# Performance work log

Measured on AMD Instinct MI355X. Metric: run time of the kernel, lower is better.

## Reference

```python
import jax, jax.numpy as jnp
import numpy as np

B, N_SIGNALS, SIGNAL_LEN, H = 512, 3, 4096, 17

def setup_inputs() -> dict:
    key = jax.random.key(0)
    ks = jax.random.split(key, 11)
    s = 1.0 / np.sqrt(H)  # torch nn.RNN init scale
    return {
        "x": jax.random.normal(ks[0], (B, N_SIGNALS, SIGNAL_LEN), jnp.float32),
        "W_ih_f": jax.random.uniform(ks[1], (H, N_SIGNALS), jnp.float32, -s, s),
        "W_hh_f": jax.random.uniform(ks[2], (H, H), jnp.float32, -s, s),
        "b_ih_f": jax.random.uniform(ks[3], (H,), jnp.float32, -s, s),
        "b_hh_f": jax.random.uniform(ks[4], (H,), jnp.float32, -s, s),
        "W_ih_b": jax.random.uniform(ks[5], (H, N_SIGNALS), jnp.float32, -s, s),
        "W_hh_b": jax.random.uniform(ks[6], (H, H), jnp.float32, -s, s),
        "b_ih_b": jax.random.uniform(ks[7], (H,), jnp.float32, -s, s),
        "b_hh_b": jax.random.uniform(ks[8], (H,), jnp.float32, -s, s),
        "conv_w": jax.random.uniform(ks[9], (2, 2 * H), jnp.float32, -1.0 / np.sqrt(2 * H), 1.0 / np.sqrt(2 * H)),
        "conv_b": jax.random.uniform(ks[10], (2,), jnp.float32, -1.0 / np.sqrt(2 * H), 1.0 / np.sqrt(2 * H)),
    }

def _run_rnn(xt, W_ih, W_hh, b_ih, b_hh):
    # xt: [B, T, C] -> hs: [B, T, H]
    pre = jnp.einsum('btc,hc->bth', xt, W_ih) + b_ih + b_hh  # precompute input projection
    def step(h, p):
        h = jnp.tanh(p + h @ W_hh.T)
        return h, h
    h0 = jnp.zeros((xt.shape[0], W_hh.shape[0]), xt.dtype)
    _, hs = jax.lax.scan(step, h0, jnp.swapaxes(pre, 0, 1))
    return jnp.swapaxes(hs, 0, 1)

def reference(x, W_ih_f, W_hh_f, b_ih_f, b_hh_f, W_ih_b, W_hh_b, b_ih_b, b_hh_b, conv_w, conv_b):
    xt = jnp.transpose(x, (0, 2, 1))  # [B, T, N_SIGNALS]
    fwd = _run_rnn(xt, W_ih_f, W_hh_f, b_ih_f, b_hh_f)                      # [B, T, H]
    bwd = _run_rnn(xt[:, ::-1], W_ih_b, W_hh_b, b_ih_b, b_hh_b)[:, ::-1]    # [B, T, H]
    out = jnp.concatenate([fwd, bwd], axis=-1)                               # [B, T, 2H]
    logits_t = jnp.einsum('bth,oh->bto', out, conv_w) + conv_b               # 1x1 conv == per-step linear
    return jnp.mean(logits_t, axis=1)                                        # [B, 2]
```

## Files before the change

### kernel.cpp

```cpp
#include <hip/hip_runtime.h>

#define BATCH 512
#define NC 3
#define TT 4096
#define HH 17
#define NBLK (TT / 4)
#define WU_BLKS 3
#define NSEQ (BATCH * 2)
#define SCALE 2.8853900817779268f

typedef __attribute__((ext_vector_type(8))) short short8;
typedef __attribute__((ext_vector_type(16))) float f32x16;

union B8 { unsigned u[4]; short8 s; };

__device__ __forceinline__ float fast_exp2(float y) {
#if __has_builtin(__builtin_amdgcn_exp2f)
    return __builtin_amdgcn_exp2f(y);
#else
    return exp2f(y);
#endif
}

__device__ __forceinline__ float fast_tanh_pre(float d) {
    float e = fast_exp2(d);
    float r = __builtin_amdgcn_rcpf(e + 1.0f);
    return fmaf(-2.0f, r, 1.0f);
}

__device__ __forceinline__ unsigned cvt_pk_bf16(float lo, float hi) {
    unsigned r;
    asm("v_cvt_pk_bf16_f32 %0, %1, %2" : "=v"(r) : "v"(lo), "v"(hi));
    return r;
}

__device__ __forceinline__ unsigned short bf16_rne(float f) {
    unsigned u = __float_as_uint(f);
    unsigned r = u + 0x7FFFu + ((u >> 16) & 1u);
    return (unsigned short)(r >> 16);
}

__global__ __launch_bounds__(256) void transpose_kernel(
    const float4* __restrict__ x4, uint4* __restrict__ w12,
    uint4* __restrict__ w0) {
    __shared__ float4 tile[NC][32][33];
    int bid = blockIdx.x;
    int tb = bid & 15;
    int tt = bid >> 4;
    int b0 = tb * 32, t40 = tt * 32;
    int jr = threadIdx.x & 31, pr = threadIdx.x >> 5;
#pragma unroll
    for (int c = 0; c < NC; ++c)
#pragma unroll
        for (int p = 0; p < 4; ++p) {
            int r = p * 8 + pr;
            tile[c][r][jr] =
                x4[(size_t)(b0 + r) * (NC * NBLK) + c * NBLK + t40 + jr];
        }
    __syncthreads();
#pragma unroll
    for (int p = 0; p < 4; ++p) {
        int j = p * 8 + pr;
        int b = jr;
        float4 c0 = tile[0][b][j];
        float4 c1 = tile[1][b][j];
        float4 c2 = tile[2][b][j];
        uint4 a, z;
        a.x = cvt_pk_bf16(c1.x, c2.x); z.x = cvt_pk_bf16(0.0f, c0.x);
        a.y = cvt_pk_bf16(c1.y, c2.y); z.y = cvt_pk_bf16(0.0f, c0.y);
        a.z = cvt_pk_bf16(c1.z, c2.z); z.z = cvt_pk_bf16(0.0f, c0.z);
        a.w = cvt_pk_bf16(c1.w, c2.w); z.w = cvt_pk_bf16(0.0f, c0.w);
        size_t idx = (size_t)(t40 + j) * BATCH + b0 + b;
        w12[idx] = a;
        w0[idx] = z;
    }
}

template <int DIR>
__device__ __forceinline__ void run_loop(
    const uint4* __restrict__ p12, const uint4* __restrict__ p0,
    short8 Ahi, short8 Alo, short8 A2hi, short8 A2lo,
    f32x16 Cb, int g, int blk0, int blkMain, int blkEnd, float* hs) {

    short8 Bhi = {0,0,0,0,0,0,0,0};
    unsigned h16b = 0;

    int t4 = DIR ? (NBLK - 1 - blk0) : blk0;
    uint4 c12 = p12[(size_t)t4 * BATCH];
    uint4 c0 = p0[(size_t)t4 * BATCH];
    const int dstep = DIR ? -1 : 1;

    for (int blk = blk0; blk < blkEnd; ++blk) {
        int nt4 = (blk + 1 < blkEnd) ? t4 + dstep : t4;
        uint4 n12 = p12[(size_t)nt4 * BATCH];
        uint4 n0 = p0[(size_t)nt4 * BATCH];

        const float flag = (blk >= blkMain) ? 1.0f : 0.0f;
        unsigned a12[4] = {c12.x, c12.y, c12.z, c12.w};
        unsigned a0[4] = {c0.x, c0.y, c0.z, c0.w};

#pragma unroll
        for (int k = 0; k < 4; ++k) {
            const int kk = DIR ? (3 - k) : k;

            unsigned t0 = h16b | a0[kk];
            unsigned t1 = a12[kk];
            if (g) { t0 = 0; t1 = 0; }
            B8 th; th.u[0] = t0; th.u[1] = t1; th.u[2] = 0; th.u[3] = 0;

            f32x16 D = __builtin_amdgcn_mfma_f32_32x32x16_bf16(Ahi, Bhi, Cb, 0, 0, 0);
            D = __builtin_amdgcn_mfma_f32_32x32x16_bf16(Alo, Bhi, D, 0, 0, 0);
            D = __builtin_amdgcn_mfma_f32_32x32x16_bf16(A2hi, th.s, D, 0, 0, 0);
            D = __builtin_amdgcn_mfma_f32_32x32x16_bf16(A2lo, th.s, D, 0, 0, 0);

            float ht[9];
#pragma unroll
            for (int r = 0; r < 9; ++r) {
                ht[r] = fast_tanh_pre(D[r]);
                hs[r] = fmaf(ht[r], flag, hs[r]);
            }
            B8 nh;
            nh.u[0] = cvt_pk_bf16(ht[0], ht[1]);
            nh.u[1] = cvt_pk_bf16(ht[2], ht[3]);
            nh.u[2] = cvt_pk_bf16(ht[4], ht[5]);
            nh.u[3] = cvt_pk_bf16(ht[6], ht[7]);
            Bhi = nh.s;
            h16b = cvt_pk_bf16(ht[8], 0.0f);
        }
        t4 = nt4;
        c12 = n12; c0 = n0;
    }
}

__global__ __launch_bounds__(256) void rnn_kernel(
    const uint4* __restrict__ w12, const uint4* __restrict__ w0,
    const float* __restrict__ W_ih_f, const float* __restrict__ W_hh_f,
    const float* __restrict__ b_ih_f, const float* __restrict__ b_hh_f,
    const float* __restrict__ W_ih_b, const float* __restrict__ W_hh_b,
    const float* __restrict__ b_ih_b, const float* __restrict__ b_hh_b,
    float* __restrict__ partial, int nchunk, int bpc) {
    int wv = threadIdx.x >> 6;
    int wid = blockIdx.x * 4 + wv;
    int chunk = wid % nchunk;
    int q = wid / nchunk;
    int dir = q & 1;
    int grp = q >> 1;
    int lane = threadIdx.x & 63;
    int n = lane & 31;
    int g = lane >> 5;
    int m = n;
    int bn = grp * 32 + n;

    const float* W_ih = dir ? W_ih_b : W_ih_f;
    const float* W_hh = dir ? W_hh_b : W_hh_f;
    const float* b_ih = dir ? b_ih_b : b_ih_f;
    const float* b_hh = dir ? b_hh_b : b_hh_f;

    short8 Ahi, Alo, A2hi, A2lo;
#pragma unroll
    for (int i = 0; i < 8; ++i) {
        int k = (i < 4) ? (4 * g + i) : (8 + 4 * g + (i - 4));
        float wv_ = (m < HH && k < HH) ? W_hh[m * HH + k] * SCALE : 0.0f;
        unsigned short hb = bf16_rne(wv_);
        float hf = __uint_as_float(((unsigned)hb) << 16);
        Ahi[i] = (short)hb;
        Alo[i] = (short)bf16_rne(wv_ - hf);
        int k2 = (i < 4) ? (16 + 4 * g + i) : (24 + 4 * g + (i - 4));
        float wv2 = 0.0f;
        if (m < HH) {
            if (k2 == 16) wv2 = W_hh[m * HH + 16] * SCALE;
            else if (k2 >= 17 && k2 <= 19) wv2 = W_ih[m * NC + (k2 - 17)] * SCALE;
        }
        unsigned short hb2 = bf16_rne(wv2);
        float hf2 = __uint_as_float(((unsigned)hb2) << 16);
        A2hi[i] = (short)hb2;
        A2lo[i] = (short)bf16_rne(wv2 - hf2);
    }

    f32x16 Cb;
#pragma unroll
    for (int r = 0; r < 16; ++r) {
        int row = (r & 3) + 8 * (r >> 2) + 4 * g;
        Cb[r] = (row < HH) ? (b_ih[row] + b_hh[row]) * SCALE : 0.0f;
    }

    int blkMain = chunk * bpc;
    int blk0 = chunk ? (blkMain - WU_BLKS) : 0;
    int blkEnd = blkMain + bpc;

    const uint4* p12 = w12 + bn;
    const uint4* p0 = w0 + bn;

    float hs[9];
#pragma unroll
    for (int r = 0; r < 9; ++r) hs[r] = 0.0f;

    if (dir == 0)
        run_loop<0>(p12, p0, Ahi, Alo, A2hi, A2lo, Cb, g, blk0, blkMain, blkEnd, hs);
    else
        run_loop<1>(p12, p0, Ahi, Alo, A2hi, A2lo, Cb, g, blk0, blkMain, blkEnd, hs);

    int seq = bn * 2 + dir;
#pragma unroll
    for (int r = 0; r < 9; ++r) {
        int row = (r & 3) + 8 * (r >> 2) + 4 * g;
        if (row < HH)
            partial[(size_t)chunk * (NSEQ * HH) + seq * HH + row] = hs[r];
    }
}

__global__ __launch_bounds__(64) void finalize_kernel(
    const float* __restrict__ partial, const float* __restrict__ conv_w,
    const float* __restrict__ conv_b, float* __restrict__ out, int nchunk) {
    int b = blockIdx.x;
    int lane = threadIdx.x;
    float tot = 0.0f;
    if (lane < 2 * HH) {
        const float* p = partial + (size_t)b * (2 * HH) + lane;
        float s0 = 0.0f, s1 = 0.0f, s2 = 0.0f, s3 = 0.0f;
        int c = 0;
        for (; c + 4 <= nchunk; c += 4) {
            s0 += p[(size_t)(c + 0) * (NSEQ * HH)];
            s1 += p[(size_t)(c + 1) * (NSEQ * HH)];
            s2 += p[(size_t)(c + 2) * (NSEQ * HH)];
            s3 += p[(size_t)(c + 3) * (NSEQ * HH)];
        }
        for (; c < nchunk; ++c) s0 += p[(size_t)c * (NSEQ * HH)];
        tot = (s0 + s1) + (s2 + s3);
    }
    float c0 = 0.0f, c1 = 0.0f;
    if (lane < 2 * HH) {
        c0 = conv_w[lane] * tot;
        c1 = conv_w[2 * HH + lane] * tot;
    }
#pragma unroll
    for (int off = 32; off; off >>= 1) {
        c0 += __shfl_down(c0, off);
        c1 += __shfl_down(c1, off);
    }
    if (lane == 0) {
        const float inv = 1.0f / (float)TT;
        out[b * 2 + 0] = fmaf(c0, inv, conv_b[0]);
        out[b * 2 + 1] = fmaf(c1, inv, conv_b[1]);
    }
}

extern "C" void kernel_launch(void* const* d_in, const int* in_sizes, int n_in,
                              void* d_out, int out_size, void* d_ws, size_t ws_size,
                              hipStream_t stream) {
    const float* x      = (const float*)d_in[0];
    const float* W_ih_f = (const float*)d_in[1];
    const float* W_hh_f = (const float*)d_in[2];
    const float* b_ih_f = (const float*)d_in[3];
    const float* b_hh_f = (const float*)d_in[4];
    const float* W_ih_b = (const float*)d_in[5];
    const float* W_hh_b = (const float*)d_in[6];
    const float* b_ih_b = (const float*)d_in[7];
    const float* b_hh_b = (const float*)d_in[8];
    const float* conv_w = (const float*)d_in[9];
    const float* conv_b = (const float*)d_in[10];

    const size_t wbytes = (size_t)NBLK * BATCH * 16;
    const size_t pbytes1 = (size_t)NSEQ * HH * 4;
    size_t pbase = 2 * wbytes;
    int nchunk = 128;
    while (nchunk > 8 && ws_size < pbase + (size_t)nchunk * pbytes1)
        nchunk >>= 1;
    int bpc = NBLK / nchunk;

    uint4* w12 = (uint4*)d_ws;
    uint4* w0 = (uint4*)((char*)d_ws + wbytes);
    float* partial = (float*)((char*)d_ws + pbase);
    float* out = (float*)d_out;

    transpose_kernel<<<dim3(16 * 32), dim3(256), 0, stream>>>(
        (const float4*)x, w12, w0);
    rnn_kernel<<<dim3(32 * nchunk / 4), dim3(256), 0, stream>>>(
        w12, w0, W_ih_f, W_hh_f, b_ih_f, b_hh_f,
        W_ih_b, W_hh_b, b_ih_b, b_hh_b, partial, nchunk, bpc);
    finalize_kernel<<<dim3(BATCH), dim3(64), 0, stream>>>(
        partial, conv_w, conv_b, out, nchunk);
}
```

Before: 62.19 us.

## Interleave two independent time chunks per wave to hide MFMA/tanh latency

Each wave now runs two time chunks (A and B, half the chunk count apart) of the same sequence in lockstep, interleaving their MFMA chains and tanh work. This gives the scheduler independent instructions to fill the serial dependency latency of the recurrence. The chunk count rises to 256, so each chunk is shorter, while the grid size stays the same. The trade-off is higher register pressure, plus a proportionally larger warm-up overhead per useful block.

```diff
diff --git a/kernel.cpp b/kernel.cpp
--- a/kernel.cpp
+++ b/kernel.cpp
@@ -77,59 +77,94 @@
 }
 
 template <int DIR>
-__device__ __forceinline__ void run_loop(
+__device__ __forceinline__ void run_pair(
     const uint4* __restrict__ p12, const uint4* __restrict__ p0,
     short8 Ahi, short8 Alo, short8 A2hi, short8 A2lo,
-    f32x16 Cb, int g, int blk0, int blkMain, int blkEnd, float* hs) {
-
-    short8 Bhi = {0,0,0,0,0,0,0,0};
-    unsigned h16b = 0;
-
-    int t4 = DIR ? (NBLK - 1 - blk0) : blk0;
-    uint4 c12 = p12[(size_t)t4 * BATCH];
-    uint4 c0 = p0[(size_t)t4 * BATCH];
-    const int dstep = DIR ? -1 : 1;
-
-    for (int blk = blk0; blk < blkEnd; ++blk) {
-        int nt4 = (blk + 1 < blkEnd) ? t4 + dstep : t4;
-        uint4 n12 = p12[(size_t)nt4 * BATCH];
-        uint4 n0 = p0[(size_t)nt4 * BATCH];
-
-        const float flag = (blk >= blkMain) ? 1.0f : 0.0f;
-        unsigned a12[4] = {c12.x, c12.y, c12.z, c12.w};
-        unsigned a0[4] = {c0.x, c0.y, c0.z, c0.w};
+    f32x16 Cb, int g, int blkMainA, int blkMainB, int bpc,
+    float* hsA, float* hsB) {
+
+    short8 BhiA = {0,0,0,0,0,0,0,0};
+    short8 BhiB = {0,0,0,0,0,0,0,0};
+    unsigned h16bA = 0, h16bB = 0;
+
+    const int T = WU_BLKS + bpc;
+    int blkA = blkMainA - WU_BLKS;
+    int blkB = blkMainB - WU_BLKS;
+    const int endA = blkMainA + bpc - 1;
+    const int endB = blkMainB + bpc - 1;
+
+#define T4OF(blk) (DIR ? (NBLK - 1 - ((blk) < 0 ? 0 : (blk))) \
+                       : ((blk) < 0 ? 0 : (blk)))
+    int t4A = T4OF(blkA), t4B = T4OF(blkB);
+    uint4 c12A = p12[(size_t)t4A * BATCH], c0A = p0[(size_t)t4A * BATCH];
+    uint4 c12B = p12[(size_t)t4B * BATCH], c0B = p0[(size_t)t4B * BATCH];
+
+    for (int i = 0; i < T; ++i) {
+        int nA = (blkA + 1 > endA) ? endA : blkA + 1;
+        int nB = (blkB + 1 > endB) ? endB : blkB + 1;
+        int t4An = T4OF(nA), t4Bn = T4OF(nB);
+        uint4 n12A = p12[(size_t)t4An * BATCH], n0A = p0[(size_t)t4An * BATCH];
+        uint4 n12B = p12[(size_t)t4Bn * BATCH], n0B = p0[(size_t)t4Bn * BATCH];
+
+        const float flagA = (blkA >= blkMainA) ? 1.0f : 0.0f;
+        const float flagB = (blkB >= blkMainB) ? 1.0f : 0.0f;
+        const bool updA = (blkA >= 0);
+
+        unsigned a12A[4] = {c12A.x, c12A.y, c12A.z, c12A.w};
+        unsigned a0A[4] = {c0A.x, c0A.y, c0A.z, c0A.w};
+        unsigned a12B[4] = {c12B.x, c12B.y, c12B.z, c12B.w};
+        unsigned a0B[4] = {c0B.x, c0B.y, c0B.z, c0B.w};
 
 #pragma unroll
         for (int k = 0; k < 4; ++k) {
             const int kk = DIR ? (3 - k) : k;
 
-            unsigned t0 = h16b | a0[kk];
-            unsigned t1 = a12[kk];
-            if (g) { t0 = 0; t1 = 0; }
-            B8 th; th.u[0] = t0; th.u[1] = t1; th.u[2] = 0; th.u[3] = 0;
-
-            f32x16 D = __builtin_amdgcn_mfma_f32_32x32x16_bf16(Ahi, Bhi, Cb, 0, 0, 0);
-            D = __builtin_amdgcn_mfma_f32_32x32x16_bf16(Alo, Bhi, D, 0, 0, 0);
-            D = __builtin_amdgcn_mfma_f32_32x32x16_bf16(A2hi, th.s, D, 0, 0, 0);
-            D = __builtin_amdgcn_mfma_f32_32x32x16_bf16(A2lo, th.s, D, 0, 0, 0);
-
-            float ht[9];
+            unsigned t0A = h16bA | a0A[kk];
+            unsigned t1A = a12A[kk];
+            unsigned t0B = h16bB | a0B[kk];
+            unsigned t1B = a12B[kk];
+            if (g) { t0A = 0; t1A = 0; t0B = 0; t1B = 0; }
+            B8 thA; thA.u[0] = t0A; thA.u[1] = t1A; thA.u[2] = 0; thA.u[3] = 0;
+            B8 thB; thB.u[0] = t0B; thB.u[1] = t1B; thB.u[2] = 0; thB.u[3] = 0;
+
+            f32x16 DA = __builtin_amdgcn_mfma_f32_32x32x16_bf16(Ahi, BhiA, Cb, 0, 0, 0);
+            f32x16 DB = __builtin_amdgcn_mfma_f32_32x32x16_bf16(Ahi, BhiB, Cb, 0, 0, 0);
+            DA = __builtin_amdgcn_mfma_f32_32x32x16_bf16(Alo, BhiA, DA, 0, 0, 0);
+            DB = __builtin_amdgcn_mfma_f32_32x32x16_bf16(Alo, BhiB, DB, 0, 0, 0);
+            DA = __builtin_amdgcn_mfma_f32_32x32x16_bf16(A2hi, thA.s, DA, 0, 0, 0);
+            DB = __builtin_amdgcn_mfma_f32_32x32x16_bf16(A2hi, thB.s, DB, 0, 0, 0);
+            DA = __builtin_amdgcn_mfma_f32_32x32x16_bf16(A2lo, thA.s, DA, 0, 0, 0);
+            DB = __builtin_amdgcn_mfma_f32_32x32x16_bf16(A2lo, thB.s, DB, 0, 0, 0);
+
+            float htA[9], htB[9];
 #pragma unroll
             for (int r = 0; r < 9; ++r) {
-                ht[r] = fast_tanh_pre(D[r]);
-                hs[r] = fmaf(ht[r], flag, hs[r]);
+                htA[r] = fast_tanh_pre(DA[r]);
+                htB[r] = fast_tanh_pre(DB[r]);
+                hsA[r] = fmaf(htA[r], flagA, hsA[r]);
+                hsB[r] = fmaf(htB[r], flagB, hsB[r]);
             }
-            B8 nh;
-            nh.u[0] = cvt_pk_bf16(ht[0], ht[1]);
-            nh.u[1] = cvt_pk_bf16(ht[2], ht[3]);
-            nh.u[2] = cvt_pk_bf16(ht[4], ht[5]);
-            nh.u[3] = cvt_pk_bf16(ht[6], ht[7]);
-            Bhi = nh.s;
-            h16b = cvt_pk_bf16(ht[8], 0.0f);
-        }
-        t4 = nt4;
-        c12 = n12; c0 = n0;
-    }
+            B8 nhA, nhB;
+            nhA.u[0] = cvt_pk_bf16(htA[0], htA[1]);
+            nhB.u[0] = cvt_pk_bf16(htB[0], htB[1]);
+            nhA.u[1] = cvt_pk_bf16(htA[2], htA[3]);
+            nhB.u[1] = cvt_pk_bf16(htB[2], htB[3]);
+            nhA.u[2] = cvt_pk_bf16(htA[4], htA[5]);
+            nhB.u[2] = cvt_pk_bf16(htB[4], htB[5]);
+            nhA.u[3] = cvt_pk_bf16(htA[6], htA[7]);
+            nhB.u[3] = cvt_pk_bf16(htB[6], htB[7]);
+            if (updA) {
+                BhiA = nhA.s;
+                h16bA = cvt_pk_bf16(htA[8], 0.0f);
+            }
+            BhiB = nhB.s;
+            h16bB = cvt_pk_bf16(htB[8], 0.0f);
+        }
+        blkA += 1; blkB += 1;
+        c12A = n12A; c0A = n0A;
+        c12B = n12B; c0B = n0B;
+    }
+#undef T4OF
 }
 
 __global__ __launch_bounds__(256) void rnn_kernel(
@@ -141,8 +176,10 @@
     float* __restrict__ partial, int nchunk, int bpc) {
     int wv = threadIdx.x >> 6;
     int wid = blockIdx.x * 4 + wv;
-    int chunk = wid % nchunk;
-    int q = wid / nchunk;
+    int half = nchunk >> 1;
+    int p = wid % half;
+    int q = wid / half;
+    int cA = p, cB = p + half;
     int dir = q & 1;
     int grp = q >> 1;
     int lane = threadIdx.x & 63;
@@ -184,28 +221,28 @@
         Cb[r] = (row < HH) ? (b_ih[row] + b_hh[row]) * SCALE : 0.0f;
     }
 
-    int blkMain = chunk * bpc;
-    int blk0 = chunk ? (blkMain - WU_BLKS) : 0;
-    int blkEnd = blkMain + bpc;
-
     const uint4* p12 = w12 + bn;
     const uint4* p0 = w0 + bn;
 
-    float hs[9];
-#pragma unroll
-    for (int r = 0; r < 9; ++r) hs[r] = 0.0f;
+    float hsA[9], hsB[9];
+#pragma unroll
+    for (int r = 0; r < 9; ++r) { hsA[r] = 0.0f; hsB[r] = 0.0f; }
 
     if (dir == 0)
-        run_loop<0>(p12, p0, Ahi, Alo, A2hi, A2lo, Cb, g, blk0, blkMain, blkEnd, hs);
+        run_pair<0>(p12, p0, Ahi, Alo, A2hi, A2lo, Cb, g,
+                    cA * bpc, cB * bpc, bpc, hsA, hsB);
     else
-        run_loop<1>(p12, p0, Ahi, Alo, A2hi, A2lo, Cb, g, blk0, blkMain, blkEnd, hs);
+        run_pair<1>(p12, p0, Ahi, Alo, A2hi, A2lo, Cb, g,
+                    cA * bpc, cB * bpc, bpc, hsA, hsB);
 
     int seq = bn * 2 + dir;
 #pragma unroll
     for (int r = 0; r < 9; ++r) {
         int row = (r & 3) + 8 * (r >> 2) + 4 * g;
-        if (row < HH)
-            partial[(size_t)chunk * (NSEQ * HH) + seq * HH + row] = hs[r];
+        if (row < HH) {
+            partial[(size_t)cA * (NSEQ * HH) + seq * HH + row] = hsA[r];
+            partial[(size_t)cB * (NSEQ * HH) + seq * HH + row] = hsB[r];
+        }
     }
 }
 
@@ -263,7 +300,7 @@
     const size_t wbytes = (size_t)NBLK * BATCH * 16;
     const size_t pbytes1 = (size_t)NSEQ * HH * 4;
     size_t pbase = 2 * wbytes;
-    int nchunk = 128;
+    int nchunk = 256;
     while (nchunk > 8 && ws_size < pbase + (size_t)nchunk * pbytes1)
         nchunk >>= 1;
     int bpc = NBLK / nchunk;
@@ -275,7 +312,7 @@
 
     transpose_kernel<<<dim3(16 * 32), dim3(256), 0, stream>>>(
         (const float4*)x, w12, w0);
-    rnn_kernel<<<dim3(32 * nchunk / 4), dim3(256), 0, stream>>>(
+    rnn_kernel<<<dim3(4 * nchunk), dim3(256), 0, stream>>>(
         w12, w0, W_ih_f, W_hh_f, b_ih_f, b_hh_f,
         W_ih_b, W_hh_b, b_ih_b, b_hh_b, partial, nchunk, bpc);
     finalize_kernel<<<dim3(BATCH), dim3(64), 0, stream>>>(
```

Measured after the change: 88.06 us. 1.42x slower.
